# Performance work log

Hardware: AMD Instinct MI355X
Metric: run time of the kernel (lower is better)

## Reference

```python
import jax, jax.numpy as jnp
import numpy as np

DT_MIN, DT_MAX, STAB_EPS, RMS_EPS = 1e-4, 10.0, 1e-8, 1e-6


def soft_clamp(x, mn=DT_MIN, mx=DT_MAX):
    center = (mx + mn) / 2.0
    half = (mx - mn) / 2.0
    return center + half * jnp.tanh((x - center) / half)


def setup_inputs() -> dict:
    key = jax.random.key(0)
    ks = jax.random.split(key, 8)
    B, L, D, N = 1, 4096, 1024, 16
    s = D ** -0.5
    x = jax.random.normal(ks[0], (B, L, D), jnp.float32)
    # S4D-real style init: A = -exp(A_log), rows = -(1..N)
    A_log = jnp.broadcast_to(jnp.log(jnp.arange(1, N + 1, dtype=jnp.float32)), (D, N))
    W_delta = jax.random.normal(ks[1], (D, D), jnp.float32) * s
    b_delta = jax.random.normal(ks[2], (D,), jnp.float32) * 0.1
    W_B = jax.random.normal(ks[3], (D, N), jnp.float32) * s
    W_C = jax.random.normal(ks[4], (D, N), jnp.float32) * s
    D_skip = jax.random.normal(ks[5], (D,), jnp.float32) * 0.1 + 1.0
    norm_weight = jnp.ones((D,), jnp.float32)
    return {"x": x, "A_log": A_log, "W_delta": W_delta, "b_delta": b_delta,
            "W_B": W_B, "W_C": W_C, "D_skip": D_skip, "norm_weight": norm_weight}


def reference(x, A_log, W_delta, b_delta, W_B, W_C, D_skip, norm_weight):
    # RMSNorm pre-norm
    rms = jnp.sqrt(jnp.mean(x * x, axis=-1, keepdims=True) + RMS_EPS)
    xn = norm_weight * x / rms                                  # (B, L, D)

    # input-dependent (selective) parameters
    delta = soft_clamp(jax.nn.softplus(xn @ W_delta + b_delta))  # (B, L, D)
    Bp = xn @ W_B                                               # (B, L, N)
    C = xn @ W_C                                                # (B, L, N)
    A = -jnp.exp(A_log)                                         # (D, N)

    # guarded Tustin (bilinear) discretization
    half_dA = 0.5 * delta[..., None] * A                        # (B, L, D, N)
    denom_inv = 1.0 / jnp.maximum(1.0 - half_dA, STAB_EPS)
    A_bar = (1.0 + half_dA) * denom_inv                         # (B, L, D, N)
    B_bar = jnp.sqrt(delta)[..., None] * Bp[:, :, None, :] * denom_inv
    Bx = B_bar * xn[..., None]                                  # (B, L, D, N)

    # linear recurrence h_t = A_bar_t * h_{t-1} + Bx_t ; y_t = sum_n C_t * h_t
    def step(h, inp):
        a_t, bx_t, c_t = inp
        h = a_t * h + bx_t                                      # (B, D, N)
        y_t = jnp.einsum('bdn,bn->bd', h, c_t)
        return h, y_t

    h0 = jnp.zeros((x.shape[0], A.shape[0], A.shape[1]), x.dtype)
    seq = (jnp.moveaxis(A_bar, 1, 0), jnp.moveaxis(Bx, 1, 0), jnp.moveaxis(C, 1, 0))
    _, ys = jax.lax.scan(step, h0, seq)
    y = jnp.moveaxis(ys, 0, 1) + D_skip * xn                    # skip connection
    return y
```

## Files before the change

kernel.cpp:

```cpp
#include <hip/hip_runtime.h>
#include <hip/hip_fp16.h>
#include <cmath>

typedef _Float16 half8 __attribute__((ext_vector_type(8)));
typedef _Float16 half4_t __attribute__((ext_vector_type(4)));
typedef float f32x4 __attribute__((ext_vector_type(4)));

#define LDIM 4096
#define DDIM 1024
#define NSTATE 16
#define NCHUNK 128
#define CLEN 32

#define GLD16(g, l) __builtin_amdgcn_global_load_lds( \
    (const __attribute__((address_space(1))) void*)(g), \
    (__attribute__((address_space(3))) void*)(l), 16, 0, 0)

__global__ __launch_bounds__(256) void k_prep_norm(const float* __restrict__ x,
                                                   const float* __restrict__ nw,
                                                   const float* __restrict__ W,
                                                   const float* __restrict__ WB,
                                                   const float* __restrict__ WC,
                                                   _Float16* __restrict__ xnh,
                                                   _Float16* __restrict__ Wt,
                                                   _Float16* __restrict__ BCe,
                                                   float* __restrict__ bpc) {
  const int b = blockIdx.x, t = threadIdx.x;
  if (b < 4096) {
    const int l = b;
    if (t < 32) bpc[(size_t)l * 32 + t] = 0.f;
    float4 v = ((const float4*)(x + (size_t)l * DDIM))[t];
    float ss = v.x * v.x + v.y * v.y + v.z * v.z + v.w * v.w;
#pragma unroll
    for (int off = 32; off; off >>= 1) ss += __shfl_xor(ss, off, 64);
    __shared__ float sred[4];
    if ((t & 63) == 0) sred[t >> 6] = ss;
    __syncthreads();
    float tot = sred[0] + sred[1] + sred[2] + sred[3];
    float r = rsqrtf(tot * (1.0f / (float)DDIM) + 1e-6f);
    float4 wv = ((const float4*)nw)[t];
    half4_t h;
    h[0] = (_Float16)(v.x * wv.x * r); h[1] = (_Float16)(v.y * wv.y * r);
    h[2] = (_Float16)(v.z * wv.z * r); h[3] = (_Float16)(v.w * wv.w * r);
    ((half4_t*)(xnh + (size_t)l * DDIM))[t] = h;
  } else if (b < 4352) {
    __shared__ float tile[64][65];
    const int bb = b - 4096;
    const int n0 = (bb & 15) * 64, k0 = (bb >> 4) * 64;
#pragma unroll
    for (int i = 0; i < 16; ++i) {
      int idx = t + i * 256;
      int kk = idx >> 6, nn = idx & 63;
      tile[kk][nn] = W[(size_t)(k0 + kk) * DDIM + n0 + nn];
    }
    __syncthreads();
#pragma unroll
    for (int i = 0; i < 16; ++i) {
      int idx = t + i * 256;
      int nn = idx >> 6, kk = idx & 63;
      Wt[(size_t)(n0 + nn) * DDIM + k0 + kk] = (_Float16)tile[kk][nn];
    }
  } else {
    const int by2 = b - 4352;
#pragma unroll
    for (int rr = 0; rr < 2; ++rr) {
      int r = 2 * by2 + rr;
      const float* src = (r & 1) ? WC : WB;
      int n = r >> 1;
#pragma unroll
      for (int j = 0; j < 4; ++j) {
        int k = t * 4 + j;
        BCe[(size_t)r * DDIM + k] = (_Float16)src[(size_t)k * NSTATE + n];
      }
    }
  }
}

__global__ __launch_bounds__(256, 2) void k_gemm64(const _Float16* __restrict__ Ah,
                                                   const _Float16* __restrict__ Bh,
                                                   const _Float16* __restrict__ B2h,
                                                   const float* __restrict__ b_delta,
                                                   _Float16* __restrict__ sdh,
                                                   float* __restrict__ bpc) {
  __shared__ __align__(16) _Float16 As[2][128 * 32];
  __shared__ __align__(16) _Float16 Bs[2][64 * 32];
  __shared__ __align__(16) _Float16 B2s[2][32 * 32];
  const int t = threadIdx.x;
  const int w = t >> 6, lane = t & 63;
  const int quad = lane >> 4, l16 = lane & 15;
  const int wr = w >> 1, wc = w & 1;
  const int bid = blockIdx.x;
  const int bx = bid & 15, by = bid >> 4;
  const int tileM = by * 128, tileN = bx * 64;
  const int srow = lane >> 2, scol = (lane & 3) * 8;
  const _Float16* gA0 = Ah + (size_t)(tileM + w * 32 + srow) * DDIM + scol;
  const _Float16* gB0 = Bh + (size_t)(tileN + w * 16 + srow) * DDIM + scol;
  const _Float16* gC0 = B2h + (size_t)(w * 16 + srow) * DDIM + scol;

  f32x4 acc[4][2], acc2[4];
#pragma unroll
  for (int i = 0; i < 4; ++i) {
    acc2[i] = (f32x4){0.f, 0.f, 0.f, 0.f};
#pragma unroll
    for (int j = 0; j < 2; ++j) acc[i][j] = (f32x4){0.f, 0.f, 0.f, 0.f};
  }

  auto stage = [&](int kt, int p) {
    const int ko = kt * 32;
    GLD16(gA0 + ko,             &As[p][(w * 32) * 32]);
    GLD16(gA0 + 16 * DDIM + ko, &As[p][(w * 32 + 16) * 32]);
    GLD16(gB0 + ko,             &Bs[p][(w * 16) * 32]);
    if ((kt >> 1) == bx && w < 2)
      GLD16(gC0 + ko,           &B2s[p][(w * 16) * 32]);
  };

  stage(0, 0);
  for (int kt = 0; kt < 32; ++kt) {
    const int p = kt & 1;
    __syncthreads();
    if (kt < 31) stage(kt + 1, p ^ 1);
    half8 af[4], bf[2];
#pragma unroll
    for (int i = 0; i < 4; ++i)
      af[i] = *(const half8*)&As[p][(wr * 64 + i * 16 + l16) * 32 + quad * 8];
#pragma unroll
    for (int j = 0; j < 2; ++j)
      bf[j] = *(const half8*)&Bs[p][(wc * 32 + j * 16 + l16) * 32 + quad * 8];
#pragma unroll
    for (int i = 0; i < 4; ++i)
#pragma unroll
      for (int j = 0; j < 2; ++j)
        acc[i][j] = __builtin_amdgcn_mfma_f32_16x16x32_f16(af[i], bf[j], acc[i][j], 0, 0, 0);
    if ((kt >> 1) == bx) {
      half8 cf = *(const half8*)&B2s[p][(wc * 16 + l16) * 32 + quad * 8];
#pragma unroll
      for (int i = 0; i < 4; ++i)
        acc2[i] = __builtin_amdgcn_mfma_f32_16x16x32_f16(af[i], cf, acc2[i], 0, 0, 0);
    }
  }

  const float cC = 5.00005f, cH = 4.99995f, invH = 1.0f / 4.99995f;
  float bdl[2];
#pragma unroll
  for (int j = 0; j < 2; ++j) bdl[j] = b_delta[tileN + wc * 32 + j * 16 + l16];
#pragma unroll
  for (int i = 0; i < 4; ++i) {
#pragma unroll
    for (int r = 0; r < 4; ++r) {
      int row = tileM + wr * 64 + i * 16 + quad * 4 + r;
#pragma unroll
      for (int j = 0; j < 2; ++j) {
        int col = tileN + wc * 32 + j * 16 + l16;
        float z = acc[i][j][r] + bdl[j];
        float e = __expf(-fabsf(z));
        float sp = fmaxf(z, 0.f) + __logf(1.0f + e);
        float tt = (sp - cC) * invH;
        float e2 = __expf(-2.0f * fabsf(tt));
        float th = copysignf((1.0f - e2) / (1.0f + e2), tt);
        float dt = fmaf(cH, th, cC);
        sdh[(size_t)row * DDIM + col] = (_Float16)sqrtf(dt);
      }
      atomicAdd(&bpc[(size_t)row * 32 + wc * 16 + l16], acc2[i][r]);
    }
  }
}

__global__ __launch_bounds__(256) void k_scan1(const _Float16* __restrict__ sdh,
                                               const _Float16* __restrict__ xnh,
                                               const float* __restrict__ bpc,
                                               const float* __restrict__ A_log,
                                               float2* __restrict__ Ph) {
  __shared__ float2 bcs[CLEN * NSTATE];
  const int t = threadIdx.x;
  const int d = blockIdx.x * 256 + t;
  const int c = blockIdx.y;
#pragma unroll
  for (int u = t; u < CLEN * NSTATE; u += 256) {
    int l = u >> 4, n2 = (u & 15) * 2;
    bcs[u] = *(const float2*)&bpc[(size_t)(c * CLEN + l) * 32 + n2];
  }
  float halfA[NSTATE], h[NSTATE], P[NSTATE];
#pragma unroll
  for (int n = 0; n < NSTATE; ++n) {
    halfA[n] = -0.5f * __expf(A_log[d * NSTATE + n]);
    h[n] = 0.f; P[n] = 1.f;
  }
  __syncthreads();
  const _Float16* sdr = sdh + (size_t)c * CLEN * DDIM + d;
  const _Float16* xr = xnh + (size_t)c * CLEN * DDIM + d;
#pragma unroll 2
  for (int i = 0; i < CLEN; ++i) {
    float sdv = (float)sdr[(size_t)i * DDIM];
    float xv = (float)xr[(size_t)i * DDIM];
    float dsq = sdv * sdv;
    float sdx = sdv * xv;
#pragma unroll
    for (int n = 0; n < NSTATE; ++n) {
      float2 bc = bcs[i * NSTATE + n];
      float hd = dsq * halfA[n];
      float di = __builtin_amdgcn_rcpf(1.0f - hd);
      float ab = fmaf(hd, di, di);
      h[n] = fmaf(ab, h[n], sdx * bc.x * di);
      P[n] *= ab;
    }
  }
#pragma unroll
  for (int n = 0; n < NSTATE; ++n)
    Ph[((size_t)c * NSTATE + n) * DDIM + d] = make_float2(P[n], h[n]);
}

__global__ __launch_bounds__(64) void k_comb(const float2* __restrict__ Ph,
                                             float* __restrict__ Hinit) {
  const int g = blockIdx.x * 64 + threadIdx.x;
  float H = 0.f;
  for (int cb = 0; cb < NCHUNK; cb += 8) {
    float2 ph[8];
#pragma unroll
    for (int u = 0; u < 8; ++u)
      ph[u] = Ph[(size_t)(cb + u) * (DDIM * NSTATE) + g];
#pragma unroll
    for (int u = 0; u < 8; ++u) {
      Hinit[(size_t)(cb + u) * (DDIM * NSTATE) + g] = H;
      H = fmaf(ph[u].x, H, ph[u].y);
    }
  }
}

__global__ __launch_bounds__(256) void k_scan2(const _Float16* __restrict__ sdh,
                                               const _Float16* __restrict__ xnh,
                                               const float* __restrict__ bpc,
                                               const float* __restrict__ A_log,
                                               const float* __restrict__ Hinit,
                                               const float* __restrict__ Dskip,
                                               float* __restrict__ y) {
  __shared__ float2 bcs[CLEN * NSTATE];
  const int t = threadIdx.x;
  const int d = blockIdx.x * 256 + t;
  const int c = blockIdx.y;
#pragma unroll
  for (int u = t; u < CLEN * NSTATE; u += 256) {
    int l = u >> 4, n2 = (u & 15) * 2;
    bcs[u] = *(const float2*)&bpc[(size_t)(c * CLEN + l) * 32 + n2];
  }
  float halfA[NSTATE], h[NSTATE];
#pragma unroll
  for (int n = 0; n < NSTATE; ++n) {
    halfA[n] = -0.5f * __expf(A_log[d * NSTATE + n]);
    h[n] = Hinit[(size_t)c * (DDIM * NSTATE) + n * DDIM + d];
  }
  const float dsk = Dskip[d];
  __syncthreads();
  const _Float16* sdr = sdh + (size_t)c * CLEN * DDIM + d;
  const _Float16* xr = xnh + (size_t)c * CLEN * DDIM + d;
  float* yr = y + (size_t)c * CLEN * DDIM + d;
#pragma unroll 2
  for (int i = 0; i < CLEN; ++i) {
    float sdv = (float)sdr[(size_t)i * DDIM];
    float xv = (float)xr[(size_t)i * DDIM];
    float dsq = sdv * sdv;
    float sdx = sdv * xv;
    float acc = dsk * xv;
#pragma unroll
    for (int n = 0; n < NSTATE; ++n) {
      float2 bc = bcs[i * NSTATE + n];
      float hd = dsq * halfA[n];
      float di = __builtin_amdgcn_rcpf(1.0f - hd);
      float ab = fmaf(hd, di, di);
      h[n] = fmaf(ab, h[n], sdx * bc.x * di);
      acc = fmaf(bc.y, h[n], acc);
    }
    yr[(size_t)i * DDIM] = acc;
  }
}

extern "C" void kernel_launch(void* const* d_in, const int* in_sizes, int n_in,
                              void* d_out, int out_size, void* d_ws, size_t ws_size,
                              hipStream_t stream) {
  const float* x       = (const float*)d_in[0];
  const float* A_log   = (const float*)d_in[1];
  const float* W_delta = (const float*)d_in[2];
  const float* b_delta = (const float*)d_in[3];
  const float* W_B     = (const float*)d_in[4];
  const float* W_C     = (const float*)d_in[5];
  const float* D_skip  = (const float*)d_in[6];
  const float* norm_w  = (const float*)d_in[7];
  float* y = (float*)d_out;

  char* ws = (char*)d_ws;
  const size_t MB = 1024 * 1024;
  _Float16* xnh = (_Float16*)(ws);
  _Float16* Wt  = (_Float16*)(ws + 8 * MB);
  _Float16* BCe = (_Float16*)(ws + 10 * MB);
  _Float16* sdh = (_Float16*)(ws + 11 * MB);
  float*    bpc = (float*)(ws + 19 * MB);
  float2*   Ph  = (float2*)(ws + 20 * MB);
  float*    Hin = (float*)(ws + 36 * MB);
  (void)ws_size; (void)in_sizes; (void)n_in; (void)out_size;

  hipLaunchKernelGGL(k_prep_norm, dim3(4368), dim3(256), 0, stream,
                     x, norm_w, W_delta, W_B, W_C, xnh, Wt, BCe, bpc);
  hipLaunchKernelGGL(k_gemm64, dim3(512), dim3(256), 0, stream,
                     xnh, Wt, BCe, b_delta, sdh, bpc);
  hipLaunchKernelGGL(k_scan1, dim3(4, NCHUNK), dim3(256), 0, stream,
                     sdh, xnh, bpc, A_log, Ph);
  hipLaunchKernelGGL(k_comb, dim3(256), dim3(64), 0, stream, Ph, Hin);
  hipLaunchKernelGGL(k_scan2, dim3(4, NCHUNK), dim3(256), 0, stream,
                     sdh, xnh, bpc, A_log, Hin, D_skip, y);
}
```

Before: 167.4 us.

## Double GEMM K-tile to 64 with XOR-swizzled LDS and single-block B/C projection

Raises the GEMM K-step from 32 to 64, which halves the number of barrier-separated iterations, and XOR-swizzles the LDS layout so the wider rows do not cause bank conflicts. The B/C projection (32 columns) is no longer spread across all column blocks with atomicAdd. Only bx==0 blocks now compute it over the full K range and write it directly, so the zeroing of bpc in the prep kernel is removed. This trades atomics and the zero-init for extra load imbalance on the bx==0 blocks and doubled LDS use, which may reduce occupancy.

```diff
diff --git a/kernel.cpp b/kernel.cpp
--- a/kernel.cpp
+++ b/kernel.cpp
@@ -23,12 +23,10 @@
                                                    const float* __restrict__ WC,
                                                    _Float16* __restrict__ xnh,
                                                    _Float16* __restrict__ Wt,
-                                                   _Float16* __restrict__ BCe,
-                                                   float* __restrict__ bpc) {
+                                                   _Float16* __restrict__ BCe) {
   const int b = blockIdx.x, t = threadIdx.x;
   if (b < 4096) {
     const int l = b;
-    if (t < 32) bpc[(size_t)l * 32 + t] = 0.f;
     float4 v = ((const float4*)(x + (size_t)l * DDIM))[t];
     float ss = v.x * v.x + v.y * v.y + v.z * v.z + v.w * v.w;
 #pragma unroll
@@ -82,9 +80,9 @@
                                                    const float* __restrict__ b_delta,
                                                    _Float16* __restrict__ sdh,
                                                    float* __restrict__ bpc) {
-  __shared__ __align__(16) _Float16 As[2][128 * 32];
-  __shared__ __align__(16) _Float16 Bs[2][64 * 32];
-  __shared__ __align__(16) _Float16 B2s[2][32 * 32];
+  __shared__ __align__(16) _Float16 As[2][128 * 64];
+  __shared__ __align__(16) _Float16 Bs[2][64 * 64];
+  __shared__ __align__(16) _Float16 B2s[2][32 * 64];
   const int t = threadIdx.x;
   const int w = t >> 6, lane = t & 63;
   const int quad = lane >> 4, l16 = lane & 15;
@@ -92,10 +90,11 @@
   const int bid = blockIdx.x;
   const int bx = bid & 15, by = bid >> 4;
   const int tileM = by * 128, tileN = bx * 64;
-  const int srow = lane >> 2, scol = (lane & 3) * 8;
-  const _Float16* gA0 = Ah + (size_t)(tileM + w * 32 + srow) * DDIM + scol;
-  const _Float16* gB0 = Bh + (size_t)(tileN + w * 16 + srow) * DDIM + scol;
-  const _Float16* gC0 = B2h + (size_t)(w * 16 + srow) * DDIM + scol;
+  const int srow = lane >> 3;
+  const int sslot = (lane & 7) ^ srow;
+  const _Float16* gA0 = Ah + (size_t)(tileM + w * 32 + srow) * DDIM + sslot * 8;
+  const _Float16* gB0 = Bh + (size_t)(tileN + w * 16 + srow) * DDIM + sslot * 8;
+  const _Float16* gC0 = B2h + (size_t)(w * 8 + srow) * DDIM + sslot * 8;
 
   f32x4 acc[4][2], acc2[4];
 #pragma unroll
@@ -106,36 +105,43 @@
   }
 
   auto stage = [&](int kt, int p) {
-    const int ko = kt * 32;
-    GLD16(gA0 + ko,             &As[p][(w * 32) * 32]);
-    GLD16(gA0 + 16 * DDIM + ko, &As[p][(w * 32 + 16) * 32]);
-    GLD16(gB0 + ko,             &Bs[p][(w * 16) * 32]);
-    if ((kt >> 1) == bx && w < 2)
-      GLD16(gC0 + ko,           &B2s[p][(w * 16) * 32]);
+    const int ko = kt * 64;
+#pragma unroll
+    for (int g = 0; g < 4; ++g)
+      GLD16(gA0 + (size_t)g * 8 * DDIM + ko, &As[p][(w * 32 + g * 8) * 64]);
+#pragma unroll
+    for (int g = 0; g < 2; ++g)
+      GLD16(gB0 + (size_t)g * 8 * DDIM + ko, &Bs[p][(w * 16 + g * 8) * 64]);
+    if (bx == 0)
+      GLD16(gC0 + ko, &B2s[p][(w * 8) * 64]);
   };
 
   stage(0, 0);
-  for (int kt = 0; kt < 32; ++kt) {
+  for (int kt = 0; kt < 16; ++kt) {
     const int p = kt & 1;
     __syncthreads();
-    if (kt < 31) stage(kt + 1, p ^ 1);
-    half8 af[4], bf[2];
-#pragma unroll
-    for (int i = 0; i < 4; ++i)
-      af[i] = *(const half8*)&As[p][(wr * 64 + i * 16 + l16) * 32 + quad * 8];
-#pragma unroll
-    for (int j = 0; j < 2; ++j)
-      bf[j] = *(const half8*)&Bs[p][(wc * 32 + j * 16 + l16) * 32 + quad * 8];
-#pragma unroll
-    for (int i = 0; i < 4; ++i)
+    if (kt < 15) stage(kt + 1, p ^ 1);
+#pragma unroll
+    for (int ks = 0; ks < 2; ++ks) {
+      const int sw = ((ks * 4 + quad) ^ (l16 & 7)) * 8;
+      half8 af[4], bf[2];
+#pragma unroll
+      for (int i = 0; i < 4; ++i)
+        af[i] = *(const half8*)&As[p][(wr * 64 + i * 16 + l16) * 64 + sw];
 #pragma unroll
       for (int j = 0; j < 2; ++j)
-        acc[i][j] = __builtin_amdgcn_mfma_f32_16x16x32_f16(af[i], bf[j], acc[i][j], 0, 0, 0);
-    if ((kt >> 1) == bx) {
-      half8 cf = *(const half8*)&B2s[p][(wc * 16 + l16) * 32 + quad * 8];
+        bf[j] = *(const half8*)&Bs[p][(wc * 32 + j * 16 + l16) * 64 + sw];
 #pragma unroll
       for (int i = 0; i < 4; ++i)
-        acc2[i] = __builtin_amdgcn_mfma_f32_16x16x32_f16(af[i], cf, acc2[i], 0, 0, 0);
+#pragma unroll
+        for (int j = 0; j < 2; ++j)
+          acc[i][j] = __builtin_amdgcn_mfma_f32_16x16x32_f16(af[i], bf[j], acc[i][j], 0, 0, 0);
+      if (bx == 0) {
+        half8 cf = *(const half8*)&B2s[p][(wc * 16 + l16) * 64 + sw];
+#pragma unroll
+        for (int i = 0; i < 4; ++i)
+          acc2[i] = __builtin_amdgcn_mfma_f32_16x16x32_f16(af[i], cf, acc2[i], 0, 0, 0);
+      }
     }
   }
 
@@ -160,7 +166,8 @@
         float dt = fmaf(cH, th, cC);
         sdh[(size_t)row * DDIM + col] = (_Float16)sqrtf(dt);
       }
-      atomicAdd(&bpc[(size_t)row * 32 + wc * 16 + l16], acc2[i][r]);
+      if (bx == 0)
+        bpc[(size_t)row * 32 + wc * 16 + l16] = acc2[i][r];
     }
   }
 }
@@ -298,7 +305,7 @@
   (void)ws_size; (void)in_sizes; (void)n_in; (void)out_size;
 
   hipLaunchKernelGGL(k_prep_norm, dim3(4368), dim3(256), 0, stream,
-                     x, norm_w, W_delta, W_B, W_C, xnh, Wt, BCe, bpc);
+                     x, norm_w, W_delta, W_B, W_C, xnh, Wt, BCe);
   hipLaunchKernelGGL(k_gemm64, dim3(512), dim3(256), 0, stream,
                      xnh, Wt, BCe, b_delta, sdh, bpc);
   hipLaunchKernelGGL(k_scan1, dim3(4, NCHUNK), dim3(256), 0, stream,
```

New measurement: 160.8 us. -3.9%, faster.
